# Kernel optimization log

Hardware: AMD Instinct MI355X
Metric: run time of the kernel (lower is better)

The kernel has to match this reference:

```python
import jax, jax.numpy as jnp
import numpy as np

START_INDEX = 1


def _lstm_cell(x, h, c, W_ih, W_hh, b_ih, b_hh):
    # PyTorch LSTM cell: gate order i, f, g, o
    gates = x @ W_ih.T + b_ih + h @ W_hh.T + b_hh  # [B, 4H]
    i, f, g, o = jnp.split(gates, 4, axis=-1)
    c_new = jax.nn.sigmoid(f) * c + jax.nn.sigmoid(i) * jnp.tanh(g)
    h_new = jax.nn.sigmoid(o) * jnp.tanh(c_new)
    return h_new, c_new


def setup_inputs() -> dict:
    key = jax.random.key(0)
    ks = jax.random.split(key, 13)
    B, C, E, H, V = 32, 512, 512, 512, 32000
    s = 0.05  # keep gates in non-saturated range

    def w(k, shape):
        return jax.random.normal(k, shape, dtype=jnp.float32) * s

    return {
        "context": jax.random.normal(ks[0], (B, C), dtype=jnp.float32),
        "emb": w(ks[1], (V, E)),
        "W_ih_l0": w(ks[2], (4 * H, E + C)),
        "W_hh_l0": w(ks[3], (4 * H, H)),
        "b_ih_l0": w(ks[4], (4 * H,)),
        "b_hh_l0": w(ks[5], (4 * H,)),
        "W_ih_l1": w(ks[6], (4 * H, H)),
        "W_hh_l1": w(ks[7], (4 * H, H)),
        "b_ih_l1": w(ks[8], (4 * H,)),
        "b_hh_l1": w(ks[9], (4 * H,)),
        "W_out": w(ks[10], (V, H)),
        "b_out": w(ks[11], (V,)),
        "max_len": 64,
    }


def reference(context, emb, W_ih_l0, W_hh_l0, b_ih_l0, b_hh_l0,
              W_ih_l1, W_hh_l1, b_ih_l1, b_hh_l1, W_out, b_out, max_len):
    B = context.shape[0]
    H = W_hh_l0.shape[1]
    tok0 = jnp.full((B,), START_INDEX, dtype=jnp.int32)
    z = jnp.zeros((B, H), dtype=context.dtype)

    def step(carry, _):
        tok, h0, c0, h1, c1 = carry
        ex = emb[tok]                                   # [B, E] embedding lookup
        inp = jnp.concatenate([ex, context], axis=-1)   # [B, E+C]
        h0, c0 = _lstm_cell(inp, h0, c0, W_ih_l0, W_hh_l0, b_ih_l0, b_hh_l0)
        h1, c1 = _lstm_cell(h0, h1, c1, W_ih_l1, W_hh_l1, b_ih_l1, b_hh_l1)
        logits = h1 @ W_out.T + b_out                   # [B, V]
        logp = jax.nn.log_softmax(logits, axis=-1)
        tok_next = jnp.argmax(logp, axis=-1).astype(jnp.int32)  # greedy feedback (detached)
        return (tok_next, h0, c0, h1, c1), logp

    _, out = jax.lax.scan(step, (tok0, z, z, z, z), None, length=max_len)
    return jnp.transpose(out, (1, 0, 2))                # [B, max_len, V]
```

## Files before the change

kernel.cpp:

```cpp
#include <hip/hip_runtime.h>
#include <math.h>

#define BB 32
#define HH 512
#define VV 32000
#define TT 64
#define NTILE 1000

#define OFF_H0T   0
#define OFF_H1T   32768
#define OFF_C0    65536
#define OFF_C1    81920
#define OFF_PC0   98304
#define OFF_AMAX  163840
#define OFF_PAIRS 163904

typedef float f32x4_ __attribute__((ext_vector_type(4)));

__device__ __forceinline__ float sigmoidf_(float x) { return 1.0f / (1.0f + expf(-x)); }

__device__ __forceinline__ float dot4(const float4 wv, const float4 xv) {
    return wv.x * xv.x + wv.y * xv.y + wv.z * xv.z + wv.w * xv.w;
}
__device__ __forceinline__ void bcast_fma(float* A, const float4 wv,
                                          const float4 x0, const float4 x1,
                                          const float4 x2, const float4 x3) {
    A[0] += wv.x * x0.x + wv.y * x1.x + wv.z * x2.x + wv.w * x3.x;
    A[1] += wv.x * x0.y + wv.y * x1.y + wv.z * x2.y + wv.w * x3.y;
    A[2] += wv.x * x0.z + wv.y * x1.z + wv.z * x2.z + wv.w * x3.z;
    A[3] += wv.x * x0.w + wv.y * x1.w + wv.z * x2.w + wv.w * x3.w;
}

__global__ void k_init(float* __restrict__ ws) {
    int idx = blockIdx.x * 256 + threadIdx.x;
    ws[OFF_H0T + idx] = 0.0f;
    ws[OFF_H1T + idx] = 0.0f;
    ws[OFF_C0 + idx]  = 0.0f;
    ws[OFF_C1 + idx]  = 0.0f;
    if (idx < BB) ((unsigned long long*)(ws + OFF_AMAX))[idx] = 0xFFFFFFFEull;
}

__global__ __launch_bounds__(256, 4) void k_pc0(
    const float* __restrict__ Wih0, const float* __restrict__ ctx,
    const float* __restrict__ bih0, const float* __restrict__ bhh0,
    float* __restrict__ pc0)
{
    __shared__ float red[16][16][32];
    const int tid = threadIdx.x;
    const int ks = tid >> 4, bg = (tid >> 2) & 3, rg = tid & 3;
    const int hu = blockIdx.x * 4 + rg;
    const int k0 = ks * 32, b0 = bg * 8;

    float acc[4][8];
#pragma unroll
    for (int g = 0; g < 4; ++g)
#pragma unroll
        for (int j = 0; j < 8; ++j) acc[g][j] = 0.0f;

    const float* wp[4];
#pragma unroll
    for (int g = 0; g < 4; ++g) wp[g] = Wih0 + (size_t)(g * 512 + hu) * 1024 + 512 + k0;

#pragma unroll 2
    for (int kk4 = 0; kk4 < 8; ++kk4) {
        const int kk = kk4 * 4;
        float4 w4[4];
#pragma unroll
        for (int g = 0; g < 4; ++g) w4[g] = *(const float4*)(wp[g] + kk);
#pragma unroll
        for (int j = 0; j < 8; ++j) {
            const float4 xe = *(const float4*)(ctx + (size_t)(b0 + j) * 512 + k0 + kk);
#pragma unroll
            for (int g = 0; g < 4; ++g) acc[g][j] += dot4(w4[g], xe);
        }
    }

#pragma unroll
    for (int g = 0; g < 4; ++g) {
        *(float4*)&red[ks][g * 4 + rg][b0]     = make_float4(acc[g][0], acc[g][1], acc[g][2], acc[g][3]);
        *(float4*)&red[ks][g * 4 + rg][b0 + 4] = make_float4(acc[g][4], acc[g][5], acc[g][6], acc[g][7]);
    }
    __syncthreads();
    if (tid < 128) {
        const int huL = (tid >> 5) & 3, b = tid & 31;
#pragma unroll
        for (int g = 0; g < 4; ++g) {
            float s = 0.0f;
#pragma unroll
            for (int k = 0; k < 16; ++k) s += red[k][g * 4 + huL][b];
            const int row = g * 512 + blockIdx.x * 4 + huL;
            pc0[(size_t)row * 32 + b] = s + bih0[row] + bhh0[row];
        }
    }
}

template <int MODE>
__global__ __launch_bounds__(256, 4) void k_lstm(
    const float* __restrict__ Wa, const float* __restrict__ Wb,
    const float* __restrict__ xA, const float* __restrict__ xB,
    const float* __restrict__ emb,
    const unsigned long long* __restrict__ amax_in,
    const float* __restrict__ pc0,
    const float* __restrict__ bih, const float* __restrict__ bhh,
    float* __restrict__ hT_out, float* __restrict__ c_st,
    unsigned long long* __restrict__ amax_reset)
{
    constexpr int SA = (MODE == 0) ? 1024 : 512;
    __shared__ float red[32][4][32];
    __shared__ float gg[4][32];

    const int tid = threadIdx.x;
    const int ks = tid >> 3, bg = tid & 7;
    const int hu = blockIdx.x;
    const int b0 = bg * 4;
    const bool partA = (ks < 16);
    const int k0 = (partA ? ks : ks - 16) * 32;

    float acc[4][4];
#pragma unroll
    for (int g = 0; g < 4; ++g)
#pragma unroll
        for (int j = 0; j < 4; ++j) acc[g][j] = 0.0f;

    const float* wp[4];
#pragma unroll
    for (int g = 0; g < 4; ++g)
        wp[g] = partA ? (Wa + (size_t)(g * 512 + hu) * SA + k0)
                      : (Wb + (size_t)(g * 512 + hu) * 512 + k0);

    const float* ep[4];
    if (MODE == 0 && partA) {
#pragma unroll
        for (int j = 0; j < 4; ++j) {
            const int tok = (int)(0xFFFFFFFFu - (unsigned)(amax_in[b0 + j] & 0xFFFFFFFFull));
            ep[j] = emb + (size_t)tok * 512 + k0;
        }
    }
    const float* xb = (partA ? xA : xB) + (size_t)k0 * 32 + b0;

#pragma unroll 4
    for (int kk4 = 0; kk4 < 8; ++kk4) {
        const int kk = kk4 * 4;
        float4 w4[4];
#pragma unroll
        for (int g = 0; g < 4; ++g) w4[g] = *(const float4*)(wp[g] + kk);
        if (MODE == 0 && partA) {
#pragma unroll
            for (int j = 0; j < 4; ++j) {
                const float4 xe = *(const float4*)(ep[j] + kk);
#pragma unroll
                for (int g = 0; g < 4; ++g) acc[g][j] += dot4(w4[g], xe);
            }
        } else {
            const float4 x0 = *(const float4*)(xb + (size_t)(kk + 0) * 32);
            const float4 x1 = *(const float4*)(xb + (size_t)(kk + 1) * 32);
            const float4 x2 = *(const float4*)(xb + (size_t)(kk + 2) * 32);
            const float4 x3 = *(const float4*)(xb + (size_t)(kk + 3) * 32);
#pragma unroll
            for (int g = 0; g < 4; ++g) bcast_fma(acc[g], w4[g], x0, x1, x2, x3);
        }
    }

#pragma unroll
    for (int g = 0; g < 4; ++g)
        *(float4*)&red[ks][g][b0] = make_float4(acc[g][0], acc[g][1], acc[g][2], acc[g][3]);
    __syncthreads();

    if (tid < 128) {
        const int g = tid >> 5, b = tid & 31;
        float s = 0.0f;
#pragma unroll
        for (int k = 0; k < 32; ++k) s += red[k][g][b];
        const int row = g * 512 + hu;
        if (MODE == 0) s += pc0[(size_t)row * 32 + b];
        else           s += bih[row] + bhh[row];
        gg[g][b] = s;
    }
    __syncthreads();

    if (tid < 32) {
        const int b = tid;
        const float gi = sigmoidf_(gg[0][b]);
        const float gf = sigmoidf_(gg[1][b]);
        const float gn = tanhf(gg[2][b]);
        const float go = sigmoidf_(gg[3][b]);
        const int ci = hu * 32 + b;
        const float cn = gf * c_st[ci] + gi * gn;
        c_st[ci] = cn;
        hT_out[ci] = go * tanhf(cn);
    }
    if (MODE == 1) {
        if (tid >= 64 && tid < 96) amax_reset[tid - 64] = 0ull;
    }
}

__global__ __launch_bounds__(256, 4) void k_logits(
    const float* __restrict__ h1T, const float* __restrict__ Wout,
    const float* __restrict__ bout, float* __restrict__ out,
    unsigned long long* __restrict__ amax, float* __restrict__ pairs, int t)
{
    __shared__ float red[8][32][35];
    __shared__ unsigned long long lmax[8][32];
    __shared__ float pm[8][32], ps[8][32];

    const int tid = threadIdx.x;
    const int rg = tid & 7, bg = (tid >> 3) & 3, ks = tid >> 5;
    const int row0 = blockIdx.x * 32 + rg * 4;
    const int b0 = bg * 8, k0 = ks * 64;

    float acc[4][8];
#pragma unroll
    for (int i = 0; i < 4; ++i)
#pragma unroll
        for (int j = 0; j < 8; ++j) acc[i][j] = 0.0f;

    const float* wp[4];
#pragma unroll
    for (int i = 0; i < 4; ++i) wp[i] = Wout + (size_t)(row0 + i) * 512 + k0;
    const float* xb = h1T + (size_t)k0 * 32 + b0;

#pragma unroll 2
    for (int kk4 = 0; kk4 < 16; ++kk4) {
        const int kk = kk4 * 4;
        const float4 x00 = *(const float4*)(xb + (size_t)(kk + 0) * 32);
        const float4 x01 = *(const float4*)(xb + (size_t)(kk + 0) * 32 + 4);
        const float4 x10 = *(const float4*)(xb + (size_t)(kk + 1) * 32);
        const float4 x11 = *(const float4*)(xb + (size_t)(kk + 1) * 32 + 4);
        const float4 x20 = *(const float4*)(xb + (size_t)(kk + 2) * 32);
        const float4 x21 = *(const float4*)(xb + (size_t)(kk + 2) * 32 + 4);
        const float4 x30 = *(const float4*)(xb + (size_t)(kk + 3) * 32);
        const float4 x31 = *(const float4*)(xb + (size_t)(kk + 3) * 32 + 4);
#pragma unroll
        for (int i = 0; i < 4; ++i) {
            const float4 w = *(const float4*)(wp[i] + kk);
            bcast_fma(&acc[i][0], w, x00, x10, x20, x30);
            bcast_fma(&acc[i][4], w, x01, x11, x21, x31);
        }
    }

#pragma unroll
    for (int i = 0; i < 4; ++i) {
        *(float4*)&red[ks][rg * 4 + i][b0]     = make_float4(acc[i][0], acc[i][1], acc[i][2], acc[i][3]);
        *(float4*)&red[ks][rg * 4 + i][b0 + 4] = make_float4(acc[i][4], acc[i][5], acc[i][6], acc[i][7]);
    }
    __syncthreads();

    {
        const int r2 = tid & 31, bq = tid >> 5;
        const int row = blockIdx.x * 32 + r2;
        const float bias = bout[row];
#pragma unroll
        for (int j = 0; j < 4; ++j) {
            const int b = bq * 4 + j;
            float v = bias;
#pragma unroll
            for (int k = 0; k < 8; ++k) v += red[k][r2][b];
            __builtin_nontemporal_store(v, out + ((size_t)b * TT + t) * VV + row);
        }
    }
    {
        const int b = tid & 31, rq = tid >> 5;
        unsigned long long best = 0ull;
        float vv[4];
#pragma unroll
        for (int i = 0; i < 4; ++i) {
            const int rr = rq * 4 + i;
            const int row = blockIdx.x * 32 + rr;
            float v = bout[row];
#pragma unroll
            for (int k = 0; k < 8; ++k) v += red[k][rr][b];
            vv[i] = v;
            unsigned u = __float_as_uint(v);
            u = (u & 0x80000000u) ? ~u : (u | 0x80000000u);
            const unsigned long long key =
                ((unsigned long long)u << 32) | (unsigned long long)(0xFFFFFFFFu - (unsigned)row);
            best = best > key ? best : key;
        }
        lmax[rq][b] = best;
        const float lm = fmaxf(fmaxf(vv[0], vv[1]), fmaxf(vv[2], vv[3]));
        ps[rq][b] = __expf(vv[0] - lm) + __expf(vv[1] - lm)
                  + __expf(vv[2] - lm) + __expf(vv[3] - lm);
        pm[rq][b] = lm;
    }
    __syncthreads();
    if (tid < 32) {
        unsigned long long bb = lmax[0][tid];
#pragma unroll
        for (int q = 1; q < 8; ++q) bb = bb > lmax[q][tid] ? bb : lmax[q][tid];
        if (bb > amax[tid]) atomicMax(&amax[tid], bb);
        if (pairs) {
            float M = pm[0][tid], S = ps[0][tid];
#pragma unroll
            for (int q = 1; q < 8; ++q) {
                const float nm = fmaxf(M, pm[q][tid]);
                S = S * __expf(M - nm) + ps[q][tid] * __expf(pm[q][tid] - nm);
                M = nm;
            }
            float* pr = pairs + ((size_t)t * NTILE + blockIdx.x) * 64;
            pr[tid] = M;
            pr[32 + tid] = S;
        }
    }
}

__global__ __launch_bounds__(256) void k_lsm(float* __restrict__ out,
                                             const float* __restrict__ pairs) {
    float* p = out + (size_t)blockIdx.x * VV;
    const int tid = threadIdx.x;
    __shared__ float sm[4], ss[4];

    float m = -1e30f, s = 0.0f;
    if (pairs) {
        const int b = blockIdx.x >> 6, t = blockIdx.x & 63;
        const float* pr = pairs + (size_t)t * NTILE * 64 + b;
        for (int tile = tid; tile < NTILE; tile += 256) {
            const float tm = pr[(size_t)tile * 64];
            const float ts = pr[(size_t)tile * 64 + 32];
            const float nm = fmaxf(m, tm);
            s = s * __expf(m - nm) + ts * __expf(tm - nm);
            m = nm;
        }
    } else {
        for (int i = tid * 4; i < VV; i += 1024) {
            const float4 v = *(const float4*)(p + i);
            const float cm = fmaxf(fmaxf(v.x, v.y), fmaxf(v.z, v.w));
            const float nm = fmaxf(m, cm);
            s = s * __expf(m - nm) + __expf(v.x - nm) + __expf(v.y - nm)
                                   + __expf(v.z - nm) + __expf(v.w - nm);
            m = nm;
        }
    }
#pragma unroll
    for (int off = 32; off > 0; off >>= 1) {
        const float om = __shfl_down(m, off, 64);
        const float os = __shfl_down(s, off, 64);
        const float nm = fmaxf(m, om);
        s = s * __expf(m - nm) + os * __expf(om - nm);
        m = nm;
    }
    if ((tid & 63) == 0) { sm[tid >> 6] = m; ss[tid >> 6] = s; }
    __syncthreads();
    float M = sm[0], S = ss[0];
#pragma unroll
    for (int w = 1; w < 4; ++w) {
        const float nm = fmaxf(M, sm[w]);
        S = S * __expf(M - nm) + ss[w] * __expf(sm[w] - nm);
        M = nm;
    }
    const float lz = M + __logf(S);
    for (int i = tid * 4; i < VV; i += 1024) {
        f32x4_ v = *(const f32x4_*)(p + i);
        v = v - lz;
        __builtin_nontemporal_store(v, (f32x4_*)(p + i));
    }
}

extern "C" void kernel_launch(void* const* d_in, const int* in_sizes, int n_in,
                              void* d_out, int out_size, void* d_ws, size_t ws_size,
                              hipStream_t stream) {
    const float* ctx  = (const float*)d_in[0];
    const float* emb  = (const float*)d_in[1];
    const float* Wih0 = (const float*)d_in[2];
    const float* Whh0 = (const float*)d_in[3];
    const float* bih0 = (const float*)d_in[4];
    const float* bhh0 = (const float*)d_in[5];
    const float* Wih1 = (const float*)d_in[6];
    const float* Whh1 = (const float*)d_in[7];
    const float* bih1 = (const float*)d_in[8];
    const float* bhh1 = (const float*)d_in[9];
    const float* Wout = (const float*)d_in[10];
    const float* bout = (const float*)d_in[11];

    float* out = (float*)d_out;
    float* ws  = (float*)d_ws;
    float* h0T[2] = { ws + OFF_H0T, ws + OFF_H0T + 16384 };
    float* h1T[2] = { ws + OFF_H1T, ws + OFF_H1T + 16384 };
    float* c0  = ws + OFF_C0;
    float* c1  = ws + OFF_C1;
    float* pc0 = ws + OFF_PC0;
    unsigned long long* amax = (unsigned long long*)(ws + OFF_AMAX);

    const size_t need_bytes = (size_t)(OFF_PAIRS + TT * NTILE * 64) * sizeof(float);
    float* pairs = (ws_size >= need_bytes) ? (ws + OFF_PAIRS) : nullptr;

    k_init<<<64, 256, 0, stream>>>(ws);
    k_pc0<<<128, 256, 0, stream>>>(Wih0, ctx, bih0, bhh0, pc0);

    for (int t = 0; t < TT; ++t) {
        const int pp = t & 1, nn = pp ^ 1;
        k_lstm<0><<<512, 256, 0, stream>>>(
            Wih0, Whh0, nullptr, h0T[pp], emb, amax, pc0, nullptr, nullptr,
            h0T[nn], c0, nullptr);
        k_lstm<1><<<512, 256, 0, stream>>>(
            Wih1, Whh1, h0T[nn], h1T[pp], emb, nullptr, nullptr, bih1, bhh1,
            h1T[nn], c1, amax);
        k_logits<<<1000, 256, 0, stream>>>(h1T[nn], Wout, bout, out, amax, pairs, t);
    }
    k_lsm<<<BB * TT, 256, 0, stream>>>(out, pairs);
}
```

Measured before the change: 5.898 ms.

## Process two hidden units per LSTM block and merge gate reduction stages

```diff
diff --git a/kernel.cpp b/kernel.cpp
--- a/kernel.cpp
+++ b/kernel.cpp
@@ -106,15 +106,14 @@
     unsigned long long* __restrict__ amax_reset)
 {
     constexpr int SA = (MODE == 0) ? 1024 : 512;
-    __shared__ float red[32][4][32];
-    __shared__ float gg[4][32];
+    __shared__ float red[16][8][32];
 
     const int tid = threadIdx.x;
-    const int ks = tid >> 3, bg = tid & 7;
-    const int hu = blockIdx.x;
+    const int ks = tid >> 4, bg = (tid >> 1) & 7, rg = tid & 1;
+    const int hu = blockIdx.x * 2 + rg;
     const int b0 = bg * 4;
-    const bool partA = (ks < 16);
-    const int k0 = (partA ? ks : ks - 16) * 32;
+    const bool partA = (ks < 8);
+    const int k0 = (partA ? ks : ks - 8) * 64;
 
     float acc[4][4];
 #pragma unroll
@@ -138,8 +137,8 @@
     }
     const float* xb = (partA ? xA : xB) + (size_t)k0 * 32 + b0;
 
-#pragma unroll 4
-    for (int kk4 = 0; kk4 < 8; ++kk4) {
+#pragma unroll 2
+    for (int kk4 = 0; kk4 < 16; ++kk4) {
         const int kk = kk4 * 4;
         float4 w4[4];
 #pragma unroll
@@ -163,29 +162,29 @@
 
 #pragma unroll
     for (int g = 0; g < 4; ++g)
-        *(float4*)&red[ks][g][b0] = make_float4(acc[g][0], acc[g][1], acc[g][2], acc[g][3]);
-    __syncthreads();
-
-    if (tid < 128) {
-        const int g = tid >> 5, b = tid & 31;
-        float s = 0.0f;
-#pragma unroll
-        for (int k = 0; k < 32; ++k) s += red[k][g][b];
-        const int row = g * 512 + hu;
-        if (MODE == 0) s += pc0[(size_t)row * 32 + b];
-        else           s += bih[row] + bhh[row];
-        gg[g][b] = s;
-    }
-    __syncthreads();
-
-    if (tid < 32) {
-        const int b = tid;
-        const float gi = sigmoidf_(gg[0][b]);
-        const float gf = sigmoidf_(gg[1][b]);
-        const float gn = tanhf(gg[2][b]);
-        const float go = sigmoidf_(gg[3][b]);
-        const int ci = hu * 32 + b;
-        const float cn = gf * c_st[ci] + gi * gn;
+        *(float4*)&red[ks][g * 2 + rg][b0] = make_float4(acc[g][0], acc[g][1], acc[g][2], acc[g][3]);
+    __syncthreads();
+
+    if (tid < 64) {
+        const int huL = tid >> 5, b = tid & 31;
+        const int hu2 = blockIdx.x * 2 + huL;
+        float gate[4];
+#pragma unroll
+        for (int g = 0; g < 4; ++g) {
+            float s = 0.0f;
+#pragma unroll
+            for (int k = 0; k < 16; ++k) s += red[k][g * 2 + huL][b];
+            const int row = g * 512 + hu2;
+            if (MODE == 0) s += pc0[(size_t)row * 32 + b];
+            else           s += bih[row] + bhh[row];
+            gate[g] = s;
+        }
+        const float gi = sigmoidf_(gate[0]);
+        const float gf = sigmoidf_(gate[1]);
+        const float gg = tanhf(gate[2]);
+        const float go = sigmoidf_(gate[3]);
+        const int ci = hu2 * 32 + b;
+        const float cn = gf * c_st[ci] + gi * gg;
         c_st[ci] = cn;
         hT_out[ci] = go * tanhf(cn);
     }
@@ -199,7 +198,7 @@
     const float* __restrict__ bout, float* __restrict__ out,
     unsigned long long* __restrict__ amax, float* __restrict__ pairs, int t)
 {
-    __shared__ float red[8][32][35];
+    __shared__ float red[8][32][36];
     __shared__ unsigned long long lmax[8][32];
     __shared__ float pm[8][32], ps[8][32];
 
@@ -255,7 +254,7 @@
             float v = bias;
 #pragma unroll
             for (int k = 0; k < 8; ++k) v += red[k][r2][b];
-            __builtin_nontemporal_store(v, out + ((size_t)b * TT + t) * VV + row);
+            out[((size_t)b * TT + t) * VV + row] = v;
         }
     }
     {
@@ -388,10 +387,10 @@
 
     for (int t = 0; t < TT; ++t) {
         const int pp = t & 1, nn = pp ^ 1;
-        k_lstm<0><<<512, 256, 0, stream>>>(
+        k_lstm<0><<<256, 256, 0, stream>>>(
             Wih0, Whh0, nullptr, h0T[pp], emb, amax, pc0, nullptr, nullptr,
             h0T[nn], c0, nullptr);
-        k_lstm<1><<<512, 256, 0, stream>>>(
+        k_lstm<1><<<256, 256, 0, stream>>>(
             Wih1, Whh1, h0T[nn], h1T[pp], emb, nullptr, nullptr, bih1, bhh1,
             h1T[nn], c1, amax);
         k_logits<<<1000, 256, 0, stream>>>(h1T[nn], Wout, bout, out, amax, pairs, t);
```

Result: faster. 5.452 ms (-7.6%).
